# Kernel optimization log

Measured on AMD Instinct MI355X. Metric: run time of the kernel, lower is better.

## Reference

```python
import jax, jax.numpy as jnp
import numpy as np
from jax import lax

NUM_LAYERS = 4
D_MODEL = 768
D_STATE = 128
D_CONV = 4
EXPAND = 2
HEADDIM = 64
D_INNER = EXPAND * D_MODEL            # 1536
NHEADS = D_INNER // HEADDIM           # 24
NGROUPS = 1
CONV_DIM = D_INNER + 2 * NGROUPS * D_STATE        # 1792 (x, B, C go through conv)
D_PROJ = 2 * D_INNER + 2 * NGROUPS * D_STATE + NHEADS  # z, xBC, dt
BATCH, SEQ = 4, 2048


def silu(x):
    return x * jax.nn.sigmoid(x)


def rmsnorm(x, w, eps):
    xf = x.astype(jnp.float32)
    var = jnp.mean(xf * xf, axis=-1, keepdims=True)
    return (w * (xf * lax.rsqrt(var + eps)).astype(x.dtype))


def ssd_scan(xh, dt, A, B, C):
    # xh: (b,s,h,p)  dt: (b,s,h)  A: (h,)  B,C: (b,s,n)
    b = xh.shape[0]
    dA = jnp.exp(dt * A)  # (b,s,h)
    # time-major for scan
    dA_s = dA.transpose(1, 0, 2)          # (s,b,h)
    dt_s = dt.transpose(1, 0, 2)          # (s,b,h)
    x_s = xh.transpose(1, 0, 2, 3)        # (s,b,h,p)
    B_s = B.transpose(1, 0, 2)            # (s,b,n)
    C_s = C.transpose(1, 0, 2)            # (s,b,n)

    h0 = jnp.zeros((b, NHEADS, HEADDIM, D_STATE), xh.dtype)

    def step(h, inp):
        dA_t, dt_t, x_t, B_t, C_t = inp
        # h_t = exp(dt*A) * h_{t-1} + dt * x outer B
        dBx = (dt_t[:, :, None, None] * x_t[:, :, :, None]) * B_t[:, None, None, :]
        h = dA_t[:, :, None, None] * h + dBx
        y = jnp.einsum('bhpn,bn->bhp', h, C_t)
        return h, y

    _, ys = lax.scan(step, h0, (dA_s, dt_s, x_s, B_s, C_s))
    return ys.transpose(1, 0, 2, 3)  # (b,s,h,p)


def mamba2_block(x, Wi, cw, cb, dtb, Alog, Dp, gw, Wo):
    b, s, _ = x.shape
    zxbcdt = jnp.einsum('bsd,ed->bse', x, Wi)  # (b,s,D_PROJ)
    z = zxbcdt[..., :D_INNER]
    xBC = zxbcdt[..., D_INNER:D_INNER + CONV_DIM]
    dt = zxbcdt[..., D_INNER + CONV_DIM:]

    # causal depthwise conv over time on (x,B,C)
    xc = xBC.transpose(0, 2, 1)  # (b, conv_dim, s)
    xc = lax.conv_general_dilated(xc, cw[:, None, :], (1,), [(D_CONV - 1, 0)],
                                  feature_group_count=CONV_DIM)
    xc = xc + cb[None, :, None]
    xBC = silu(xc.transpose(0, 2, 1))

    x_ssm = xBC[..., :D_INNER]
    Bm = xBC[..., D_INNER:D_INNER + D_STATE]
    Cm = xBC[..., D_INNER + D_STATE:]

    dt = jax.nn.softplus(dt + dtb)           # (b,s,h)
    A = -jnp.exp(Alog)                       # (h,)
    xh = x_ssm.reshape(b, s, NHEADS, HEADDIM)

    y = ssd_scan(xh, dt, A, Bm, Cm) + Dp[None, None, :, None] * xh
    y = y.reshape(b, s, D_INNER)
    y = y * silu(z)                          # gated
    y = rmsnorm(y, gw, 1e-5)
    return jnp.einsum('bse,de->bsd', y, Wo)


def setup_inputs() -> dict:
    key = jax.random.key(0)
    ks = jax.random.split(key, 12)
    L = NUM_LAYERS
    sc_in = 1.0 / np.sqrt(D_MODEL)
    sc_out = 1.0 / np.sqrt(D_INNER)
    sc_conv = np.sqrt(2.0 / D_CONV)
    u = jax.random.uniform(ks[5], (L, NHEADS), minval=1e-3, maxval=0.1)
    return {
        'x': jax.random.normal(ks[0], (BATCH, SEQ, D_MODEL), jnp.float32),
        'in_proj_w': jax.random.normal(ks[1], (L, D_PROJ, D_MODEL), jnp.float32) * sc_in,
        'conv_w': jax.random.normal(ks[2], (L, CONV_DIM, D_CONV), jnp.float32) * sc_conv,
        'conv_b': jnp.zeros((L, CONV_DIM), jnp.float32),
        'dt_bias': jnp.log(jnp.expm1(u)),
        'A_log': jnp.log(jax.random.uniform(ks[6], (L, NHEADS), minval=1.0, maxval=16.0)),
        'D_skip': jnp.ones((L, NHEADS), jnp.float32),
        'gnorm_w': jnp.ones((L, D_INNER), jnp.float32),
        'out_proj_w': jax.random.normal(ks[7], (L, D_MODEL, D_INNER), jnp.float32) * sc_out,
        'ln_w': jnp.ones((L, D_MODEL), jnp.float32),
        'final_ln_w': jnp.ones((D_MODEL,), jnp.float32),
    }


def reference(x, in_proj_w, conv_w, conv_b, dt_bias, A_log, D_skip, gnorm_w,
              out_proj_w, ln_w, final_ln_w):
    for l in range(NUM_LAYERS):
        residual = x
        h = rmsnorm(x, ln_w[l], 1e-6)
        h = mamba2_block(h, in_proj_w[l], conv_w[l], conv_b[l], dt_bias[l],
                         A_log[l], D_skip[l], gnorm_w[l], out_proj_w[l])
        x = h + residual
    return rmsnorm(x, final_ln_w, 1e-6)
```

## Files before the change

kernel.cpp:

```cpp
#include <hip/hip_runtime.h>
#include <hip/hip_bf16.h>
#include <math.h>

#define NUM_LAYERS 4
#define D_MODEL 768
#define D_STATE 128
#define D_CONV 4
#define HEADDIM 64
#define D_INNER 1536
#define NHEADS 24
#define CONV_DIM 1792
#define D_PROJ 3352
#define BATCH 4
#define SEQ 2048
#define NROWS (BATCH*SEQ)
#define CHUNK 128
#define NCHUNK (SEQ/CHUNK)
#define LOG2E 1.4426950408889634f

typedef __bf16 bf16x8 __attribute__((ext_vector_type(8)));
typedef float f32x4 __attribute__((ext_vector_type(4)));

#define GLL(gsrc, ldst)                                                        \
  __builtin_amdgcn_global_load_lds(                                            \
      (const __attribute__((address_space(1))) unsigned int*)(gsrc),           \
      (__attribute__((address_space(3))) unsigned int*)(ldst), 16, 0, 0)

__device__ __forceinline__ float warp_reduce_sum(float v) {
  v += __shfl_xor(v, 32);
  v += __shfl_xor(v, 16);
  v += __shfl_xor(v, 8);
  v += __shfl_xor(v, 4);
  v += __shfl_xor(v, 2);
  v += __shfl_xor(v, 1);
  return v;
}

__device__ __forceinline__ float softplusf(float x) {
  return (x > 20.f) ? x : log1pf(expf(x));
}
__device__ __forceinline__ float siluf(float x) {
  return x / (1.f + expf(-x));
}

__device__ __forceinline__ void store_val(float v, float* p) { *p = v; }
__device__ __forceinline__ void store_val(float v, __hip_bfloat16* p) {
  *p = __float2bfloat16(v);
}

__global__ __launch_bounds__(256) void f32_to_bf16_kernel(
    const float* __restrict__ in, __hip_bfloat16* __restrict__ out, size_t n) {
  for (size_t i = ((size_t)blockIdx.x * 256 + threadIdx.x) * 4; i < n;
       i += (size_t)gridDim.x * 256 * 4) {
    float4 v = *(const float4*)(in + i);
    __hip_bfloat16 h0 = __float2bfloat16(v.x), h1 = __float2bfloat16(v.y);
    __hip_bfloat16 h2 = __float2bfloat16(v.z), h3 = __float2bfloat16(v.w);
    ushort4 u;
    u.x = *(unsigned short*)&h0; u.y = *(unsigned short*)&h1;
    u.z = *(unsigned short*)&h2; u.w = *(unsigned short*)&h3;
    *(ushort4*)(out + i) = u;
  }
}

template <typename OUT>
__global__ __launch_bounds__(256) void rmsnorm768_kernel(
    const float* __restrict__ in, const float* __restrict__ w,
    OUT* __restrict__ out, float eps) {
  int row = blockIdx.x;
  const float* x = in + (size_t)row * D_MODEL;
  OUT* o = out + (size_t)row * D_MODEL;
  int t = threadIdx.x;
  float v0 = x[t], v1 = x[t + 256], v2 = x[t + 512];
  float ss = v0 * v0 + v1 * v1 + v2 * v2;
  __shared__ float sred[4];
  ss = warp_reduce_sum(ss);
  if ((t & 63) == 0) sred[t >> 6] = ss;
  __syncthreads();
  float tot = sred[0] + sred[1] + sred[2] + sred[3];
  float inv = rsqrtf(tot / (float)D_MODEL + eps);
  store_val(w[t] * v0 * inv, o + t);
  store_val(w[t + 256] * v1 * inv, o + t + 256);
  store_val(w[t + 512] * v2 * inv, o + t + 512);
}

#define GEMM_PROLOGUE_AND_MAINLOOP(Asrc, Wsrc, Kdim)                           \
  int t = threadIdx.x;                                                         \
  int w = t >> 6, l = t & 63;                                                  \
  int NT = (Kdim) >> 5;                                                        \
  int ldsA0 = (w * 64) * 8;                                                    \
  int ldsA1 = (256 + w * 64) * 8;                                              \
  int lr = l & 15, lk = l >> 4;                                                \
  int wr = w >> 1, wc = w & 1;                                                 \
  int aoff = (lk * 128 + wr * 64 + lr) * 8;                                    \
  int boff = (lk * 128 + wc * 64 + lr) * 8;                                    \
  f32x4 acc[4][4];                                                             \
  _Pragma("unroll") for (int i = 0; i < 4; i++)                                \
      _Pragma("unroll") for (int j = 0; j < 4; j++) acc[i][j] = (f32x4)0.f;    \
  STAGE(0, 0);                                                                 \
  for (int kt = 0; kt < NT; ++kt) {                                            \
    int cur = kt & 1;                                                          \
    if (kt + 1 < NT) {                                                         \
      STAGE(cur ^ 1, (kt + 1) * 32);                                           \
      asm volatile("s_waitcnt vmcnt(4)" ::: "memory");                         \
    } else {                                                                   \
      asm volatile("s_waitcnt vmcnt(0)" ::: "memory");                         \
    }                                                                          \
    __builtin_amdgcn_sched_barrier(0);                                         \
    __builtin_amdgcn_s_barrier();                                              \
    __builtin_amdgcn_sched_barrier(0);                                         \
    bf16x8 av[4], bv[4];                                                       \
    _Pragma("unroll") for (int mi = 0; mi < 4; mi++)                           \
        av[mi] = *(const bf16x8*)&At[cur][aoff + mi * 128];                    \
    _Pragma("unroll") for (int ni = 0; ni < 4; ni++)                           \
        bv[ni] = *(const bf16x8*)&Bt[cur][boff + ni * 128];                    \
    __builtin_amdgcn_s_setprio(1);                                             \
    _Pragma("unroll") for (int mi = 0; mi < 4; mi++)                           \
        _Pragma("unroll") for (int ni = 0; ni < 4; ni++)                       \
            acc[mi][ni] = __builtin_amdgcn_mfma_f32_16x16x32_bf16(             \
                av[mi], bv[ni], acc[mi][ni], 0, 0, 0);                         \
    __builtin_amdgcn_s_setprio(0);                                             \
    __builtin_amdgcn_sched_barrier(0);                                         \
    __builtin_amdgcn_s_barrier();                                              \
  }

#define STAGE(buf, kofs)                                                       \
  do {                                                                         \
    GLL(Aptr + (kofs), &At[buf][ldsA0]);                                       \
    GLL(Aptr + (kofs) + 16, &At[buf][ldsA1]);                                  \
    GLL(Wptr + (kofs), &Bt[buf][ldsA0]);                                       \
    GLL(Wptr + (kofs) + 16, &Bt[buf][ldsA1]);                                  \
  } while (0)

__global__ __launch_bounds__(256) void gemm_bf16_kernel(
    const __hip_bfloat16* __restrict__ A, const __hip_bfloat16* __restrict__ W,
    const float* __restrict__ res, float* __restrict__ C,
    int M, int N, int K) {
  __shared__ __bf16 At[2][4096];
  __shared__ __bf16 Bt[2][4096];
  int cpx = gridDim.x >> 3;
  int bid = blockIdx.x;
  int bid2 = (bid & 7) * cpx + (bid >> 3);
  int nbn = (N + 127) >> 7;
  int bn = bid2 % nbn;
  int bm = bid2 / nbn;
  int m0 = bm * 128, n0 = bn * 128;
  int srow = threadIdx.x & 127;
  int kbase = (threadIdx.x >> 7) * 8;
  const __hip_bfloat16* Aptr = A + (size_t)(m0 + srow) * K + kbase;
  int nrow = n0 + srow; if (nrow >= N) nrow = N - 1;
  const __hip_bfloat16* Wptr = W + (size_t)nrow * K + kbase;

  GEMM_PROLOGUE_AND_MAINLOOP(A, W, K)

  int rbase = (l >> 4) * 4;
#pragma unroll
  for (int ni = 0; ni < 4; ni++) {
    int n = n0 + wc * 64 + ni * 16 + (l & 15);
    if (n >= N) continue;
#pragma unroll
    for (int mi = 0; mi < 4; mi++) {
#pragma unroll
      for (int r = 0; r < 4; r++) {
        int m = m0 + wr * 64 + mi * 16 + rbase + r;
        float v = acc[mi][ni][r];
        if (res) v += res[(size_t)m * N + n];
        C[(size_t)m * N + n] = v;
      }
    }
  }
}

__global__ __launch_bounds__(512, 1) void gemm_inproj_kernel(
    const __hip_bfloat16* __restrict__ A, const __hip_bfloat16* __restrict__ W,
    __hip_bfloat16* __restrict__ zout, __hip_bfloat16* __restrict__ xout,
    float* __restrict__ dtout) {
  const int K = D_MODEL, N = D_PROJ;
  __shared__ __bf16 ring[3][16384];
  int cpx = gridDim.x >> 3;
  int bid = blockIdx.x;
  int bid2 = (bid & 7) * cpx + (bid >> 3);
  int bn = bid2 % 14;
  int bm = bid2 / 14;
  int m0 = bm * 256, n0 = bn * 256;
  int t = threadIdx.x;
  int w = t >> 6, l = t & 63;
  int lr = l & 15, lk = l >> 4;
  int wr = w >> 2, wc = w & 3;

  const __hip_bfloat16* Aptr[2];
  const __hip_bfloat16* Wptr[2];
  int dOff[2];
#pragma unroll
  for (int i = 0; i < 2; i++) {
    int idx = i * 8 + w;
    int oct = idx >> 2, rb = idx & 3;
    dOff[i] = oct * 2048 + rb * 512;
    Aptr[i] = A + (size_t)(m0 + rb * 64 + l) * K + oct * 8;
    int wrow = n0 + rb * 64 + l; if (wrow >= N) wrow = N - 1;
    Wptr[i] = W + (size_t)wrow * K + oct * 8;
  }

#define PH_END()                                                              \
  do {                                                                        \
    __builtin_amdgcn_sched_barrier(0);                                        \
    __builtin_amdgcn_s_barrier();                                             \
    __builtin_amdgcn_sched_barrier(0);                                        \
  } while (0)
#define MFMA4(ACCROW, BV)                                                     \
  do {                                                                        \
    __builtin_amdgcn_s_setprio(1);                                            \
    _Pragma("unroll") for (int mi = 0; mi < 4; mi++)                          \
        acc[(ACCROW) + mi][ci] = __builtin_amdgcn_mfma_f32_16x16x32_bf16(     \
            ((ACCROW) ? av1 : av0)[mi], (BV), acc[(ACCROW) + mi][ci], 0, 0, 0);\
    __builtin_amdgcn_s_setprio(0);                                            \
  } while (0)

  f32x4 acc[8][4];
#pragma unroll
  for (int i = 0; i < 8; i++)
#pragma unroll
    for (int j = 0; j < 4; j++) acc[i][j] = (f32x4)0.f;

  const int NT = 24;
#pragma unroll
  for (int i = 0; i < 2; i++) {
    GLL(Aptr[i], &ring[0][dOff[i]]);
    GLL(Wptr[i], &ring[0][8192 + dOff[i]]);
  }
#pragma unroll
  for (int i = 0; i < 2; i++) {
    GLL(Aptr[i] + 32, &ring[1][dOff[i]]);
    GLL(Wptr[i] + 32, &ring[1][8192 + dOff[i]]);
  }

  for (int kt = 0; kt < NT; ++kt) {
    int s = kt % 3;
    int sn = (kt + 2) % 3;
    bool pf = (kt + 2) < NT;
    if (kt + 1 < NT) {
      asm volatile("s_waitcnt vmcnt(4)" ::: "memory");
    } else {
      asm volatile("s_waitcnt vmcnt(0)" ::: "memory");
    }
    PH_END();

    const __bf16* Ab = &ring[s][0];
    const __bf16* Bb = &ring[s][8192];
    bf16x8 av0[4], av1[4], bv0, bv1, bv2, bv3;
    int ci;
    if (pf) GLL(Aptr[0] + (kt + 2) * 32, &ring[sn][dOff[0]]);
#pragma unroll
    for (int mi = 0; mi < 4; mi++)
      av0[mi] = *(const bf16x8*)&Ab[lk * 2048 + (wr * 128 + mi * 16 + lr) * 8];
    bv0 = *(const bf16x8*)&Bb[lk * 2048 + (wc * 64 + 0 * 16 + lr) * 8];
    ci = 0; MFMA4(0, bv0);
    PH_END();
    if (pf) GLL(Aptr[1] + (kt + 2) * 32, &ring[sn][dOff[1]]);
    bv1 = *(const bf16x8*)&Bb[lk * 2048 + (wc * 64 + 1 * 16 + lr) * 8];
    ci = 1; MFMA4(0, bv1);
    PH_END();
    if (pf) GLL(Wptr[0] + (kt + 2) * 32, &ring[sn][8192 + dOff[0]]);
    bv2 = *(const bf16x8*)&Bb[lk * 2048 + (wc * 64 + 2 * 16 + lr) * 8];
    ci = 2; MFMA4(0, bv2);
    PH_END();
    if (pf) GLL(Wptr[1] + (kt + 2) * 32, &ring[sn][8192 + dOff[1]]);
    bv3 = *(const bf16x8*)&Bb[lk * 2048 + (wc * 64 + 3 * 16 + lr) * 8];
    ci = 3; MFMA4(0, bv3);
    PH_END();
#pragma unroll
    for (int mi = 0; mi < 4; mi++)
      av1[mi] = *(const bf16x8*)&Ab[lk * 2048 + (wr * 128 + (mi + 4) * 16 + lr) * 8];
    ci = 3; MFMA4(4, bv3);
    PH_END();
    ci = 2; MFMA4(4, bv2);
    PH_END();
    ci = 1; MFMA4(4, bv1);
    PH_END();
    ci = 0; MFMA4(4, bv0);
    PH_END();
  }
#undef PH_END
#undef MFMA4

  int rbase = lk * 4;
  if (bn < 6) {
#pragma unroll
    for (int ni = 0; ni < 4; ni++) {
      int n = n0 + wc * 64 + ni * 16 + lr;
#pragma unroll
      for (int mi = 0; mi < 8; mi++)
#pragma unroll
        for (int r = 0; r < 4; r++) {
          int m = m0 + wr * 128 + mi * 16 + rbase + r;
          zout[(size_t)m * D_INNER + n] = __float2bfloat16(acc[mi][ni][r]);
        }
    }
  } else if (bn < 13) {
    int nb = n0 - D_INNER;
#pragma unroll
    for (int ni = 0; ni < 4; ni++) {
      int n = nb + wc * 64 + ni * 16 + lr;
#pragma unroll
      for (int mi = 0; mi < 8; mi++)
#pragma unroll
        for (int r = 0; r < 4; r++) {
          int m = m0 + wr * 128 + mi * 16 + rbase + r;
          xout[(size_t)m * CONV_DIM + n] = __float2bfloat16(acc[mi][ni][r]);
        }
    }
  } else {
#pragma unroll
    for (int ni = 0; ni < 4; ni++) {
      int loc = wc * 64 + ni * 16 + lr;
      if (loc >= 24) continue;
#pragma unroll
      for (int mi = 0; mi < 8; mi++)
#pragma unroll
        for (int r = 0; r < 4; r++) {
          int m = m0 + wr * 128 + mi * 16 + rbase + r;
          dtout[(size_t)m * 24 + loc] = acc[mi][ni][r];
        }
    }
  }
}

__global__ __launch_bounds__(128) void dt_kernel(
    const float* __restrict__ dtraw, const float* __restrict__ dt_bias,
    const float* __restrict__ A_log, float* __restrict__ dtbuf,
    float* __restrict__ cum2buf) {
  int c = blockIdx.x & 15;
  int h = (blockIdx.x >> 4) % NHEADS;
  int b = blockIdx.x / (16 * NHEADS);
  int t = threadIdx.x;
  int s = c * CHUNK + t;
  float Ah = -expf(A_log[h]);
  float raw = dtraw[((size_t)b * SEQ + s) * 24 + h] + dt_bias[h];
  float dt = softplusf(raw);
  __shared__ float sc[128];
  sc[t] = dt * Ah;
  __syncthreads();
  for (int off = 1; off < 128; off <<= 1) {
    float v = (t >= off) ? sc[t - off] : 0.f;
    __syncthreads();
    sc[t] += v;
    __syncthreads();
  }
  size_t o = ((size_t)b * NHEADS + h) * SEQ + s;
  dtbuf[o] = dt;
  cum2buf[o] = sc[t] * LOG2E;
}

__global__ __launch_bounds__(256) void conv_tiles_kernel(
    const __hip_bfloat16* __restrict__ xbc, const float* __restrict__ cw,
    const float* __restrict__ cb, __hip_bfloat16* __restrict__ xA,
    __hip_bfloat16* __restrict__ Bkt, __hip_bfloat16* __restrict__ Bkn,
    __hip_bfloat16* __restrict__ Ckn) {
  __shared__ float srows[11 * CONV_DIM];
  int to = blockIdx.x & 15;
  int c  = (blockIdx.x >> 4) & 15;
  int b  = blockIdx.x >> 8;
  int t  = threadIdx.x;
  int sb = c * CHUNK + to * 8;
  const __hip_bfloat16* base = xbc + (size_t)b * SEQ * CONV_DIM;
  for (int e = t; e < 11 * 224; e += 256) {
    int r = e / 224, c8 = (e - r * 224) * 8;
    int s = sb - 3 + r;
    float* dst = &srows[r * CONV_DIM + c8];
    if (s >= 0) {
      bf16x8 v = *(const bf16x8*)&base[(size_t)s * CONV_DIM + c8];
#pragma unroll
      for (int j = 0; j < 8; j++) dst[j] = (float)v[j];
    } else {
#pragma unroll
      for (int j = 0; j < 8; j++) dst[j] = 0.f;
    }
  }
  __syncthreads();
  int bc = b * 16 + c;
#pragma unroll
  for (int k7 = 0; k7 < 7; k7++) {
    int ch = t + k7 * 256;
    float w0 = cw[ch * 4], w1 = cw[ch * 4 + 1];
    float w2 = cw[ch * 4 + 2], w3 = cw[ch * 4 + 3];
    float bias = cb[ch];
    float out[8];
#pragma unroll
    for (int j = 0; j < 8; j++) {
      float a = bias;
      a = fmaf(srows[(j + 0) * CONV_DIM + ch], w0, a);
      a = fmaf(srows[(j + 1) * CONV_DIM + ch], w1, a);
      a = fmaf(srows[(j + 2) * CONV_DIM + ch], w2, a);
      a = fmaf(srows[(j + 3) * CONV_DIM + ch], w3, a);
      out[j] = siluf(a);
    }
    if (ch < D_INNER) {
      int h = ch >> 6, p = ch & 63;
      bf16x8 v;
#pragma unroll
      for (int j = 0; j < 8; j++) v[j] = (__bf16)out[j];
      *(bf16x8*)&xA[((((size_t)bc * 24 + h) * 16 + to) * 64 + p) * 8] = v;
    } else if (ch < D_INNER + D_STATE) {
      int n = ch - D_INNER;
      bf16x8 v;
#pragma unroll
      for (int j = 0; j < 8; j++) v[j] = (__bf16)out[j];
      *(bf16x8*)&Bkt[(((size_t)bc * 16 + to) * 128 + n) * 8] = v;
      __hip_bfloat16* dst = Bkn + (size_t)bc * 16384 + ((n >> 3) * 128) * 8 + (n & 7);
#pragma unroll
      for (int j = 0; j < 8; j++)
        dst[(to * 8 + j) * 8] = __float2bfloat16(out[j]);
    } else {
      int n = ch - D_INNER - D_STATE;
      __hip_bfloat16* dst = Ckn + (size_t)bc * 16384 + ((n >> 3) * 128) * 8 + (n & 7);
#pragma unroll
      for (int j = 0; j < 8; j++)
        dst[(to * 8 + j) * 8] = __float2bfloat16(out[j]);
    }
  }
}

__global__ __launch_bounds__(256) void ssd_state_kernel(
    const __hip_bfloat16* __restrict__ xA, const __hip_bfloat16* __restrict__ Bkt,
    const float* __restrict__ dtbuf, const float* __restrict__ cum2buf,
    __hip_bfloat16* __restrict__ states) {
  __shared__ __bf16 sX[8192];
  __shared__ __bf16 sB[16384];
  __shared__ float swdt[128];
  int c = blockIdx.x & 15;
  int h = (blockIdx.x >> 4) % NHEADS;
  int b = blockIdx.x / (16 * NHEADS);
  int t = threadIdx.x;
  int l = t & 63, w = t >> 6;
  const __hip_bfloat16* xsrc = xA + ((size_t)(b * 16 + c) * 24 + h) * 8192;
  const __hip_bfloat16* bsrc = Bkt + (size_t)(b * 16 + c) * 16384;
#pragma unroll
  for (int i = 0; i < 4; i++) GLL(xsrc + (i * 256 + t) * 8, &sX[(i * 256 + t) * 8]);
#pragma unroll
  for (int i = 0; i < 8; i++) GLL(bsrc + (i * 256 + t) * 8, &sB[(i * 256 + t) * 8]);
  {
    size_t dto = ((size_t)b * NHEADS + h) * SEQ + c * CHUNK;
    if (t < 128) {
      float total2 = cum2buf[dto + 127];
      swdt[t] = dtbuf[dto + t] * exp2f(total2 - cum2buf[dto + t]);
    }
  }
  __syncthreads();
#pragma unroll
  for (int i = 0; i < 4; i++) {
    int o = i * 256 + t;
    int to = o >> 6;
    bf16x8 v = *(bf16x8*)&sX[o * 8];
#pragma unroll
    for (int j = 0; j < 8; j++)
      v[j] = (__bf16)((float)v[j] * swdt[to * 8 + j]);
    *(bf16x8*)&sX[o * 8] = v;
  }
  __syncthreads();
  int n0w = w * 32;
  f32x4 acc[4][2];
#pragma unroll
  for (int i = 0; i < 4; i++)
#pragma unroll
    for (int j = 0; j < 2; j++) acc[i][j] = (f32x4)0.f;
#pragma unroll
  for (int kk = 0; kk < 4; kk++) {
    int ko = kk * 4 + (l >> 4);
    bf16x8 av[4], bv[2];
#pragma unroll
    for (int mi = 0; mi < 4; mi++)
      av[mi] = *(const bf16x8*)&sX[(ko * 64 + mi * 16 + (l & 15)) * 8];
#pragma unroll
    for (int ni = 0; ni < 2; ni++)
      bv[ni] = *(const bf16x8*)&sB[(ko * 128 + n0w + ni * 16 + (l & 15)) * 8];
#pragma unroll
    for (int mi = 0; mi < 4; mi++)
#pragma unroll
      for (int ni = 0; ni < 2; ni++)
        acc[mi][ni] = __builtin_amdgcn_mfma_f32_16x16x32_bf16(
            av[mi], bv[ni], acc[mi][ni], 0, 0, 0);
  }
  __hip_bfloat16* dst = states + (((size_t)b * NHEADS + h) * 16 + c) * 8192;
#pragma unroll
  for (int mi = 0; mi < 4; mi++)
#pragma unroll
    for (int ni = 0; ni < 2; ni++) {
      int n = n0w + ni * 16 + (l & 15);
#pragma unroll
      for (int r = 0; r < 4; r++) {
        int p = mi * 16 + (l >> 4) * 4 + r;
        dst[((n >> 3) * 64 + p) * 8 + (n & 7)] = __float2bfloat16(acc[mi][ni][r]);
      }
    }
}

__global__ __launch_bounds__(256) void ssd_chunkscan_kernel(
    __hip_bfloat16* __restrict__ states, const float* __restrict__ cum2buf) {
  int q = blockIdx.x & 3;
  int bh = blockIdx.x >> 2;
  int t = threadIdx.x;
  int o = q * 256 + t;
  __hip_bfloat16* base = states + (size_t)bh * NCHUNK * 8192 + (size_t)o * 8;
  const float* c2 = cum2buf + (size_t)bh * SEQ;
  float hacc[8];
#pragma unroll
  for (int j = 0; j < 8; j++) hacc[j] = 0.f;
  for (int c = 0; c < NCHUNK; c++) {
    float eA = exp2f(c2[c * 128 + 127]);
    __hip_bfloat16* p = base + (size_t)c * 8192;
    bf16x8 v = *(bf16x8*)p;
    bf16x8 wv;
#pragma unroll
    for (int j = 0; j < 8; j++) {
      float tmp = (float)v[j];
      wv[j] = (__bf16)hacc[j];
      hacc[j] = fmaf(eA, hacc[j], tmp);
    }
    *(bf16x8*)p = wv;
  }
}

__global__ __launch_bounds__(256) void ssd_output_kernel(
    const __hip_bfloat16* __restrict__ Ckn, const __hip_bfloat16* __restrict__ Bkn,
    const __hip_bfloat16* __restrict__ xA, const __hip_bfloat16* __restrict__ states,
    const float* __restrict__ dtbuf, const float* __restrict__ cum2buf,
    const float* __restrict__ D_skip, __hip_bfloat16* __restrict__ y) {
  __shared__ __bf16 sC[16384];
  __shared__ __bf16 sBS[16384];
  __shared__ __bf16 sXH[8192];
  int c = blockIdx.x & 15;
  int h = (blockIdx.x >> 4) % NHEADS;
  int b = blockIdx.x / (16 * NHEADS);
  int t = threadIdx.x;
  int l = t & 63, w = t >> 6;
  int bc = b * 16 + c;
  const __hip_bfloat16* csrc = Ckn + (size_t)bc * 16384;
  const __hip_bfloat16* bsrc = Bkn + (size_t)bc * 16384;
  const __hip_bfloat16* xsrc = xA + ((size_t)bc * 24 + h) * 8192;
#pragma unroll
  for (int i = 0; i < 8; i++) GLL(csrc + (i * 256 + t) * 8, &sC[(i * 256 + t) * 8]);
#pragma unroll
  for (int i = 0; i < 8; i++) GLL(bsrc + (i * 256 + t) * 8, &sBS[(i * 256 + t) * 8]);
#pragma unroll
  for (int i = 0; i < 4; i++) GLL(xsrc + (i * 256 + t) * 8, &sXH[(i * 256 + t) * 8]);

  size_t dto = ((size_t)b * NHEADS + h) * SEQ + c * CHUNK;
  float cum2_t[8], cum2_tau[8], dt_tau[8];
#pragma unroll
  for (int fm = 0; fm < 2; fm++)
#pragma unroll
    for (int r = 0; r < 4; r++)
      cum2_t[fm * 4 + r] = cum2buf[dto + w * 32 + fm * 16 + (l >> 4) * 4 + r];
#pragma unroll
  for (int fc = 0; fc < 8; fc++) {
    cum2_tau[fc] = cum2buf[dto + fc * 16 + (l & 15)];
    dt_tau[fc] = dtbuf[dto + fc * 16 + (l & 15)];
  }
  float Dh = D_skip[h];
  __syncthreads();

  f32x4 g[2][8];
#pragma unroll
  for (int i = 0; i < 2; i++)
#pragma unroll
    for (int j = 0; j < 8; j++) g[i][j] = (f32x4)0.f;
#pragma unroll
  for (int kk = 0; kk < 4; kk++) {
    int ko = kk * 4 + (l >> 4);
    bf16x8 a0 = *(const bf16x8*)&sC[(ko * 128 + w * 32 + (l & 15)) * 8];
    bf16x8 a1 = *(const bf16x8*)&sC[(ko * 128 + w * 32 + 16 + (l & 15)) * 8];
#pragma unroll
    for (int fc = 0; fc < 8; fc++) {
      bf16x8 bv = *(const bf16x8*)&sBS[(ko * 128 + fc * 16 + (l & 15)) * 8];
      g[0][fc] = __builtin_amdgcn_mfma_f32_16x16x32_bf16(a0, bv, g[0][fc], 0, 0, 0);
      g[1][fc] = __builtin_amdgcn_mfma_f32_16x16x32_bf16(a1, bv, g[1][fc], 0, 0, 0);
    }
  }
  __syncthreads();

#pragma unroll
  for (int fm = 0; fm < 2; fm++)
#pragma unroll
    for (int fc = 0; fc < 8; fc++) {
      int tau = fc * 16 + (l & 15);
#pragma unroll
      for (int r = 0; r < 4; r++) {
        int tt = w * 32 + fm * 16 + (l >> 4) * 4 + r;
        float v = 0.f;
        if (tt >= tau) {
          v = exp2f(cum2_t[fm * 4 + r] - cum2_tau[fc]) * dt_tau[fc] * g[fm][fc][r];
          if (tt == tau) v += Dh;
        }
        sBS[((tau >> 3) * 128 + tt) * 8 + (tau & 7)] = (__bf16)v;
      }
    }
  f32x4 y1[2][4];
#pragma unroll
  for (int i = 0; i < 2; i++)
#pragma unroll
    for (int j = 0; j < 4; j++) y1[i][j] = (f32x4)0.f;
#pragma unroll
  for (int kk = 0; kk < 4; kk++) {
    int ko = kk * 4 + (l >> 4);
    bf16x8 a0 = *(const bf16x8*)&sBS[(ko * 128 + w * 32 + (l & 15)) * 8];
    bf16x8 a1 = *(const bf16x8*)&sBS[(ko * 128 + w * 32 + 16 + (l & 15)) * 8];
#pragma unroll
    for (int fc = 0; fc < 4; fc++) {
      bf16x8 bv = *(const bf16x8*)&sXH[(ko * 64 + fc * 16 + (l & 15)) * 8];
      y1[0][fc] = __builtin_amdgcn_mfma_f32_16x16x32_bf16(a0, bv, y1[0][fc], 0, 0, 0);
      y1[1][fc] = __builtin_amdgcn_mfma_f32_16x16x32_bf16(a1, bv, y1[1][fc], 0, 0, 0);
    }
  }
  __syncthreads();
  const __hip_bfloat16* hsrc = states + (((size_t)b * NHEADS + h) * 16 + c) * 8192;
#pragma unroll
  for (int i = 0; i < 4; i++) GLL(hsrc + (i * 256 + t) * 8, &sXH[(i * 256 + t) * 8]);
  __syncthreads();

  f32x4 y2[2][4];
#pragma unroll
  for (int i = 0; i < 2; i++)
#pragma unroll
    for (int j = 0; j < 4; j++) y2[i][j] = (f32x4)0.f;
#pragma unroll
  for (int kk = 0; kk < 4; kk++) {
    int ko = kk * 4 + (l >> 4);
    bf16x8 a0 = *(const bf16x8*)&sC[(ko * 128 + w * 32 + (l & 15)) * 8];
    bf16x8 a1 = *(const bf16x8*)&sC[(ko * 128 + w * 32 + 16 + (l & 15)) * 8];
#pragma unroll
    for (int fc = 0; fc < 4; fc++) {
      bf16x8 bv = *(const bf16x8*)&sXH[(ko * 64 + fc * 16 + (l & 15)) * 8];
      y2[0][fc] = __builtin_amdgcn_mfma_f32_16x16x32_bf16(a0, bv, y2[0][fc], 0, 0, 0);
      y2[1][fc] = __builtin_amdgcn_mfma_f32_16x16x32_bf16(a1, bv, y2[1][fc], 0, 0, 0);
    }
  }

  __hip_bfloat16* yr = y + ((size_t)b * SEQ + c * CHUNK) * D_INNER + h * 64;
#pragma unroll
  for (int fm = 0; fm < 2; fm++)
#pragma unroll
    for (int r = 0; r < 4; r++) {
      int tt = w * 32 + fm * 16 + (l >> 4) * 4 + r;
      float sdec = exp2f(cum2_t[fm * 4 + r]);
#pragma unroll
      for (int fc = 0; fc < 4; fc++) {
        int p = fc * 16 + (l & 15);
        yr[(size_t)tt * D_INNER + p] =
            __float2bfloat16(y1[fm][fc][r] + sdec * y2[fm][fc][r]);
      }
    }
}

__global__ __launch_bounds__(192) void gate_norm_kernel(
    __hip_bfloat16* __restrict__ y, const __hip_bfloat16* __restrict__ z,
    const float* __restrict__ gw) {
  int row = blockIdx.x;
  const __hip_bfloat16* zr = z + (size_t)row * D_INNER;
  __hip_bfloat16* yr = y + (size_t)row * D_INNER;
  int t = threadIdx.x;
  bf16x8 yv = *(const bf16x8*)&yr[t * 8];
  bf16x8 zv = *(const bf16x8*)&zr[t * 8];
  float vals[8];
  float ss = 0.f;
#pragma unroll
  for (int j = 0; j < 8; j++) {
    float zf = (float)zv[j];
    float v = (float)yv[j] * siluf(zf);
    vals[j] = v;
    ss += v * v;
  }
  __shared__ float sred[3];
  ss = warp_reduce_sum(ss);
  if ((t & 63) == 0) sred[t >> 6] = ss;
  __syncthreads();
  float tot = sred[0] + sred[1] + sred[2];
  float inv = rsqrtf(tot / (float)D_INNER + 1e-5f);
  bf16x8 o;
#pragma unroll
  for (int j = 0; j < 8; j++)
    o[j] = (__bf16)(gw[t * 8 + j] * vals[j] * inv);
  *(bf16x8*)&yr[t * 8] = o;
}

extern "C" void kernel_launch(void* const* d_in, const int* in_sizes, int n_in,
                              void* d_out, int out_size, void* d_ws, size_t ws_size,
                              hipStream_t stream) {
  const float* x          = (const float*)d_in[0];
  const float* in_proj_w  = (const float*)d_in[1];
  const float* conv_w     = (const float*)d_in[2];
  const float* conv_b     = (const float*)d_in[3];
  const float* dt_bias    = (const float*)d_in[4];
  const float* A_log      = (const float*)d_in[5];
  const float* D_skip     = (const float*)d_in[6];
  const float* gnorm_w    = (const float*)d_in[7];
  const float* out_proj_w = (const float*)d_in[8];
  const float* ln_w       = (const float*)d_in[9];
  const float* final_ln_w = (const float*)d_in[10];

  float* ws = (float*)d_ws;
  float* curx   = ws; ws += (size_t)NROWS * D_MODEL;
  float* dtraw  = ws; ws += (size_t)NROWS * 24;
  float* dtbuf  = ws; ws += (size_t)BATCH * NHEADS * SEQ;
  float* cum2   = ws; ws += (size_t)BATCH * NHEADS * SEQ;
  __hip_bfloat16* zbuf   = (__hip_bfloat16*)ws; ws += (size_t)NROWS * D_INNER / 2;
  __hip_bfloat16* xbcbuf = (__hip_bfloat16*)ws; ws += (size_t)NROWS * CONV_DIM / 2;
  __hip_bfloat16* hbuf_b = (__hip_bfloat16*)ws; ws += (size_t)NROWS * D_MODEL / 2;
  __hip_bfloat16* ybuf_b = (__hip_bfloat16*)ws; ws += (size_t)NROWS * D_INNER / 2;
  __hip_bfloat16* wi_b   = (__hip_bfloat16*)ws; ws += (size_t)NUM_LAYERS * D_PROJ * D_MODEL / 2;
  __hip_bfloat16* wo_b   = (__hip_bfloat16*)ws; ws += (size_t)NUM_LAYERS * D_MODEL * D_INNER / 2;
  __hip_bfloat16* xAb    = (__hip_bfloat16*)ws; ws += (size_t)BATCH * NCHUNK * 24 * 8192 / 2;
  __hip_bfloat16* Bkt    = (__hip_bfloat16*)ws; ws += (size_t)BATCH * NCHUNK * 16384 / 2;
  __hip_bfloat16* Bkn    = (__hip_bfloat16*)ws; ws += (size_t)BATCH * NCHUNK * 16384 / 2;
  __hip_bfloat16* Ckn    = (__hip_bfloat16*)ws; ws += (size_t)BATCH * NCHUNK * 16384 / 2;
  __hip_bfloat16* states = (__hip_bfloat16*)ws;

  f32_to_bf16_kernel<<<1024, 256, 0, stream>>>(
      in_proj_w, wi_b, (size_t)NUM_LAYERS * D_PROJ * D_MODEL);
  f32_to_bf16_kernel<<<1024, 256, 0, stream>>>(
      out_proj_w, wo_b, (size_t)NUM_LAYERS * D_MODEL * D_INNER);

  for (int l = 0; l < NUM_LAYERS; l++) {
    const float* xin = (l == 0) ? x : curx;
    rmsnorm768_kernel<__hip_bfloat16><<<NROWS, 256, 0, stream>>>(
        xin, ln_w + (size_t)l * D_MODEL, hbuf_b, 1e-6f);

    gemm_inproj_kernel<<<448, 512, 0, stream>>>(
        hbuf_b, wi_b + (size_t)l * D_PROJ * D_MODEL, zbuf, xbcbuf, dtraw);

    dt_kernel<<<BATCH * NHEADS * NCHUNK, 128, 0, stream>>>(
        dtraw, dt_bias + l * NHEADS, A_log + l * NHEADS, dtbuf, cum2);

    conv_tiles_kernel<<<BATCH * NCHUNK * 16, 256, 0, stream>>>(
        xbcbuf, conv_w + (size_t)l * CONV_DIM * D_CONV,
        conv_b + (size_t)l * CONV_DIM, xAb, Bkt, Bkn, Ckn);

    ssd_state_kernel<<<BATCH * NHEADS * NCHUNK, 256, 0, stream>>>(
        xAb, Bkt, dtbuf, cum2, states);

    ssd_chunkscan_kernel<<<BATCH * NHEADS * 4, 256, 0, stream>>>(states, cum2);

    ssd_output_kernel<<<BATCH * NHEADS * NCHUNK, 256, 0, stream>>>(
        Ckn, Bkn, xAb, states, dtbuf, cum2, D_skip + l * NHEADS, ybuf_b);

    gate_norm_kernel<<<NROWS, 192, 0, stream>>>(
        ybuf_b, zbuf, gnorm_w + (size_t)l * D_INNER);

    gemm_bf16_kernel<<<64 * 6, 256, 0, stream>>>(
        ybuf_b, wo_b + (size_t)l * D_MODEL * D_INNER, xin, curx,
        NROWS, D_MODEL, D_INNER);
  }
  rmsnorm768_kernel<float><<<NROWS, 256, 0, stream>>>(
      curx, final_ln_w, (float*)d_out, 1e-6f);
}
```

Measured before the change: 1.009 ms.

## Use triple-buffered LDS ring with interleaved loads in generic bf16 GEMM

Replaces the double-buffered main loop of the generic bf16 GEMM (used for out_proj with residual) with a three-stage LDS ring that prefetches two K-tiles ahead. The global-to-LDS loads are spread across four MFMA phases separated by barriers, mirroring the in-proj kernel's schedule. The goal is better hiding of memory latency behind MFMA work. In exchange it uses more LDS per block, which may lower occupancy, and adds extra barriers per K-step.

Result: no change. 1.023 ms (+1.3%).

```diff
diff --git a/kernel.cpp b/kernel.cpp
--- a/kernel.cpp
+++ b/kernel.cpp
@@ -83,60 +83,18 @@
   store_val(w[t + 512] * v2 * inv, o + t + 512);
 }
 
-#define GEMM_PROLOGUE_AND_MAINLOOP(Asrc, Wsrc, Kdim)                           \
-  int t = threadIdx.x;                                                         \
-  int w = t >> 6, l = t & 63;                                                  \
-  int NT = (Kdim) >> 5;                                                        \
-  int ldsA0 = (w * 64) * 8;                                                    \
-  int ldsA1 = (256 + w * 64) * 8;                                              \
-  int lr = l & 15, lk = l >> 4;                                                \
-  int wr = w >> 1, wc = w & 1;                                                 \
-  int aoff = (lk * 128 + wr * 64 + lr) * 8;                                    \
-  int boff = (lk * 128 + wc * 64 + lr) * 8;                                    \
-  f32x4 acc[4][4];                                                             \
-  _Pragma("unroll") for (int i = 0; i < 4; i++)                                \
-      _Pragma("unroll") for (int j = 0; j < 4; j++) acc[i][j] = (f32x4)0.f;    \
-  STAGE(0, 0);                                                                 \
-  for (int kt = 0; kt < NT; ++kt) {                                            \
-    int cur = kt & 1;                                                          \
-    if (kt + 1 < NT) {                                                         \
-      STAGE(cur ^ 1, (kt + 1) * 32);                                           \
-      asm volatile("s_waitcnt vmcnt(4)" ::: "memory");                         \
-    } else {                                                                   \
-      asm volatile("s_waitcnt vmcnt(0)" ::: "memory");                         \
-    }                                                                          \
-    __builtin_amdgcn_sched_barrier(0);                                         \
-    __builtin_amdgcn_s_barrier();                                              \
-    __builtin_amdgcn_sched_barrier(0);                                         \
-    bf16x8 av[4], bv[4];                                                       \
-    _Pragma("unroll") for (int mi = 0; mi < 4; mi++)                           \
-        av[mi] = *(const bf16x8*)&At[cur][aoff + mi * 128];                    \
-    _Pragma("unroll") for (int ni = 0; ni < 4; ni++)                           \
-        bv[ni] = *(const bf16x8*)&Bt[cur][boff + ni * 128];                    \
-    __builtin_amdgcn_s_setprio(1);                                             \
-    _Pragma("unroll") for (int mi = 0; mi < 4; mi++)                           \
-        _Pragma("unroll") for (int ni = 0; ni < 4; ni++)                       \
-            acc[mi][ni] = __builtin_amdgcn_mfma_f32_16x16x32_bf16(             \
-                av[mi], bv[ni], acc[mi][ni], 0, 0, 0);                         \
-    __builtin_amdgcn_s_setprio(0);                                             \
-    __builtin_amdgcn_sched_barrier(0);                                         \
-    __builtin_amdgcn_s_barrier();                                              \
-  }
-
-#define STAGE(buf, kofs)                                                       \
-  do {                                                                         \
-    GLL(Aptr + (kofs), &At[buf][ldsA0]);                                       \
-    GLL(Aptr + (kofs) + 16, &At[buf][ldsA1]);                                  \
-    GLL(Wptr + (kofs), &Bt[buf][ldsA0]);                                       \
-    GLL(Wptr + (kofs) + 16, &Bt[buf][ldsA1]);                                  \
+#define PH_END()                                                              \
+  do {                                                                        \
+    __builtin_amdgcn_sched_barrier(0);                                        \
+    __builtin_amdgcn_s_barrier();                                             \
+    __builtin_amdgcn_sched_barrier(0);                                        \
   } while (0)
 
 __global__ __launch_bounds__(256) void gemm_bf16_kernel(
     const __hip_bfloat16* __restrict__ A, const __hip_bfloat16* __restrict__ W,
     const float* __restrict__ res, float* __restrict__ C,
     int M, int N, int K) {
-  __shared__ __bf16 At[2][4096];
-  __shared__ __bf16 Bt[2][4096];
+  __shared__ __bf16 ring[3][8192];
   int cpx = gridDim.x >> 3;
   int bid = blockIdx.x;
   int bid2 = (bid & 7) * cpx + (bid >> 3);
@@ -144,18 +102,85 @@
   int bn = bid2 % nbn;
   int bm = bid2 / nbn;
   int m0 = bm * 128, n0 = bn * 128;
-  int srow = threadIdx.x & 127;
-  int kbase = (threadIdx.x >> 7) * 8;
+  int t = threadIdx.x;
+  int w = t >> 6, l = t & 63;
+  int srow = t & 127;
+  int kbase = (t >> 7) * 8;
   const __hip_bfloat16* Aptr = A + (size_t)(m0 + srow) * K + kbase;
   int nrow = n0 + srow; if (nrow >= N) nrow = N - 1;
   const __hip_bfloat16* Wptr = W + (size_t)nrow * K + kbase;
-
-  GEMM_PROLOGUE_AND_MAINLOOP(A, W, K)
-
-  int rbase = (l >> 4) * 4;
+  int ldsA0 = (w * 64) * 8;
+  int ldsA1 = (256 + w * 64) * 8;
+  int lr = l & 15, lk = l >> 4;
+  int wr = w >> 1, wc = w & 1;
+  int aoff = (lk * 128 + wr * 64 + lr) * 8;
+  int boff = (lk * 128 + wc * 64 + lr) * 8;
+
+#define MFMA4C(CI, BV)                                                        \
+  do {                                                                        \
+    __builtin_amdgcn_s_setprio(1);                                            \
+    _Pragma("unroll") for (int mi = 0; mi < 4; mi++)                          \
+        acc[mi][CI] = __builtin_amdgcn_mfma_f32_16x16x32_bf16(                \
+            av[mi], (BV), acc[mi][CI], 0, 0, 0);                              \
+    __builtin_amdgcn_s_setprio(0);                                            \
+  } while (0)
+
+  f32x4 acc[4][4];
+#pragma unroll
+  for (int i = 0; i < 4; i++)
+#pragma unroll
+    for (int j = 0; j < 4; j++) acc[i][j] = (f32x4)0.f;
+
+  int NT = K >> 5;
+  GLL(Aptr, &ring[0][ldsA0]);
+  GLL(Aptr + 16, &ring[0][ldsA1]);
+  GLL(Wptr, &ring[0][4096 + ldsA0]);
+  GLL(Wptr + 16, &ring[0][4096 + ldsA1]);
+  GLL(Aptr + 32, &ring[1][ldsA0]);
+  GLL(Aptr + 48, &ring[1][ldsA1]);
+  GLL(Wptr + 32, &ring[1][4096 + ldsA0]);
+  GLL(Wptr + 48, &ring[1][4096 + ldsA1]);
+
+  for (int kt = 0; kt < NT; ++kt) {
+    int s = kt % 3;
+    int sn = (kt + 2) % 3;
+    bool pf = (kt + 2) < NT;
+    if (kt + 1 < NT) {
+      asm volatile("s_waitcnt vmcnt(4)" ::: "memory");
+    } else {
+      asm volatile("s_waitcnt vmcnt(0)" ::: "memory");
+    }
+    PH_END();
+
+    const __bf16* Ab = &ring[s][0];
+    const __bf16* Bb = &ring[s][4096];
+    bf16x8 av[4], bv0, bv1, bv2, bv3;
+    if (pf) GLL(Aptr + (kt + 2) * 32, &ring[sn][ldsA0]);
+#pragma unroll
+    for (int mi = 0; mi < 4; mi++)
+      av[mi] = *(const bf16x8*)&Ab[aoff + mi * 128];
+    bv0 = *(const bf16x8*)&Bb[boff + 0 * 128];
+    MFMA4C(0, bv0);
+    PH_END();
+    if (pf) GLL(Aptr + (kt + 2) * 32 + 16, &ring[sn][ldsA1]);
+    bv1 = *(const bf16x8*)&Bb[boff + 1 * 128];
+    MFMA4C(1, bv1);
+    PH_END();
+    if (pf) GLL(Wptr + (kt + 2) * 32, &ring[sn][4096 + ldsA0]);
+    bv2 = *(const bf16x8*)&Bb[boff + 2 * 128];
+    MFMA4C(2, bv2);
+    PH_END();
+    if (pf) GLL(Wptr + (kt + 2) * 32 + 16, &ring[sn][4096 + ldsA1]);
+    bv3 = *(const bf16x8*)&Bb[boff + 3 * 128];
+    MFMA4C(3, bv3);
+    PH_END();
+  }
+#undef MFMA4C
+
+  int rbase = lk * 4;
 #pragma unroll
   for (int ni = 0; ni < 4; ni++) {
-    int n = n0 + wc * 64 + ni * 16 + (l & 15);
+    int n = n0 + wc * 64 + ni * 16 + lr;
     if (n >= N) continue;
 #pragma unroll
     for (int mi = 0; mi < 4; mi++) {
@@ -200,12 +225,6 @@
     Wptr[i] = W + (size_t)wrow * K + oct * 8;
   }
 
-#define PH_END()                                                              \
-  do {                                                                        \
-    __builtin_amdgcn_sched_barrier(0);                                        \
-    __builtin_amdgcn_s_barrier();                                             \
-    __builtin_amdgcn_sched_barrier(0);                                        \
-  } while (0)
 #define MFMA4(ACCROW, BV)                                                     \
   do {                                                                        \
     __builtin_amdgcn_s_setprio(1);                                            \
@@ -279,7 +298,6 @@
     ci = 0; MFMA4(4, bv0);
     PH_END();
   }
-#undef PH_END
 #undef MFMA4
 
   int rbase = lk * 4;
```
